# Optimization experiments

Hardware: AMD Instinct MI355X
Metric: run time of the kernel (lower is better)

Reference implementation:

```python
import jax, jax.numpy as jnp
import numpy as np

P, D, K, E, ITERS, THRESH, NCLS = 16, 384, 16, 8, 10, 0.9, 1000


def _forward(x, pw, pb, ln_g, ln_b, pos, qw, qb, kw, kb, vw, vb,
             ew, eb, nw, nb, m1w, m1b, m2w, m2b, fbw, fbb, fgw, fgb, cw, cb):
    B, C, H, W = x.shape
    Hp, Wp = H // P, W // P
    # patch embedding: conv(k=s=P) == reshape + matmul; (c, ph, pw) ordering matches conv weight layout
    xp = x.reshape(B, C, Hp, P, Wp, P).transpose(0, 2, 4, 1, 3, 5).reshape(B, Hp * Wp, C * P * P)
    patches = xp @ pw + pb                                    # [B, N, D]
    # layer norm (eps=1e-5)
    mu = patches.mean(-1, keepdims=True)
    var = patches.var(-1, keepdims=True)
    pn = (patches - mu) / jnp.sqrt(var + 1e-5) * ln_g + ln_b
    # k-means (Lloyd, fixed iters, deterministic evenly-spaced init)
    N = pn.shape[1]
    init_idx = jnp.linspace(0, N - 1, K).astype(jnp.int32)
    centers0 = pn[:, init_idx]                                # [B, K, D]
    pn_sq = jnp.sum(pn * pn, -1)                              # [B, N]

    def kstep(centers, _):
        d2 = (pn_sq[:, :, None]
              - 2.0 * jnp.einsum('bnd,bkd->bnk', pn, centers)
              + jnp.sum(centers * centers, -1)[:, None, :])   # [B, N, K]
        oh = jax.nn.one_hot(jnp.argmin(d2, -1), K, dtype=pn.dtype)
        counts = oh.sum(1)                                    # [B, K]
        new = jnp.einsum('bnk,bnd->bkd', oh, pn) / jnp.maximum(counts, 1.0)[:, :, None]
        new = jnp.where(counts[:, :, None] > 0, new, centers)
        return new, None

    clusters, _ = jax.lax.scan(kstep, centers0, None, length=ITERS)  # [B, K, D]
    # attention over clusters
    clusters = clusters + pos
    Q = clusters @ qw + qb
    Kt = clusters @ kw + kb
    V = clusters @ vw + vb
    attn = jax.nn.softmax(jnp.einsum('bqd,bkd->bqk', Q, Kt) / jnp.sqrt(jnp.float32(D)), -1)
    clusters = jnp.einsum('bqk,bkd->bqd', attn, V)
    # hypergraph laplacian
    hw = jax.nn.softmax(clusters @ ew + eb, axis=1)           # [B, K, E], softmax over nodes
    Dd = hw.sum(1)                                            # [B, E]
    Hm = hw.transpose(0, 2, 1)                                # [B, E, K]
    M = (Dd ** -0.5)[:, :, None] * Hm                         # D^{-1/2} H
    L = jnp.eye(E, dtype=clusters.dtype) - jnp.einsum('bek,bfk->bef', M, Hm)  # [B, E, E]
    L = jnp.pad(L, ((0, 0), (0, K - E), (0, K - E)))          # pad to [B, K, K]
    clusters = jnp.einsum('bij,bjd->bid', L, clusters)
    clusters = clusters @ nw + nb
    # non-linear propagation MLP (exact GELU, torch default)
    clusters = jax.nn.gelu(clusters @ m1w + m1b, approximate=False) @ m2w + m2b
    # adaptive node collapse: mask from ORIGINAL clusters, sequential in-place merges
    nrm = jnp.maximum(jnp.linalg.norm(clusters, axis=-1, keepdims=True), 1e-12)
    nc = clusters / nrm
    sim = jnp.einsum('bqd,bkd->bqk', nc, nc)
    mask_any = jnp.any(sim > THRESH, axis=0)                  # [K, K]: merge pair if ANY batch exceeds
    for i in range(K):                                        # small fixed K; matches sequential torch loop
        for j in range(i + 1, K):
            cond = mask_any[i, j]
            merged = (clusters[:, i] + clusters[:, j]) * 0.5
            clusters = clusters.at[:, i].set(jnp.where(cond, merged, clusters[:, i]))
            clusters = clusters.at[:, j].set(jnp.where(cond, merged, clusters[:, j]))
    # feedback modulation
    g = clusters.mean(1)                                      # [B, D]
    fb = g @ fbw + fbb
    gate = jax.nn.sigmoid(g @ fgw + fgb)                      # [B, 1]
    clusters = clusters + fb[:, None, :] * gate[:, None, :]
    return clusters.reshape(B, -1) @ cw + cb                  # [B, num_classes]


def setup_inputs() -> dict:
    key = jax.random.key(0)
    ks = jax.random.split(key, 16)
    Wm = lambda k, *s: jax.random.normal(k, s, jnp.float32) * 0.02
    z = lambda *s: jnp.zeros(s, jnp.float32)
    return {
        'x': jax.random.normal(ks[0], (128, 3, 224, 224), jnp.float32),
        'pw': Wm(ks[1], 3 * P * P, D), 'pb': z(D),
        'ln_g': jnp.ones((D,), jnp.float32), 'ln_b': z(D),
        'pos': Wm(ks[2], K, D),
        'qw': Wm(ks[3], D, D), 'qb': z(D),
        'kw': Wm(ks[4], D, D), 'kb': z(D),
        'vw': Wm(ks[5], D, D), 'vb': z(D),
        'ew': Wm(ks[6], D, E), 'eb': z(E),
        'nw': Wm(ks[7], D, D), 'nb': z(D),
        'm1w': Wm(ks[8], D, D), 'm1b': z(D),
        'm2w': Wm(ks[9], D, D), 'm2b': z(D),
        'fbw': Wm(ks[10], D, D), 'fbb': z(D),
        'fgw': Wm(ks[11], D, 1), 'fgb': z(1),
        'cw': Wm(ks[12], D * K, NCLS), 'cb': z(NCLS),
    }


def reference(x, pw, pb, ln_g, ln_b, pos, qw, qb, kw, kb, vw, vb,
              ew, eb, nw, nb, m1w, m1b, m2w, m2b, fbw, fbb, fgw, fgb, cw, cb):
    return _forward(x, pw, pb, ln_g, ln_b, pos, qw, qb, kw, kb, vw, vb,
                    ew, eb, nw, nb, m1w, m1b, m2w, m2b, fbw, fbb, fgw, fgb, cw, cb)
```

## Files before the change

### kernel.cpp

```cpp
#include <hip/hip_runtime.h>
#include <math.h>

#define NBATCH 128
#define NPTS   196
#define DIN    768
#define DM     384
#define KCL    16
#define NEXP   8
#define NITER  10
#define NCLS   1000

__global__ __launch_bounds__(256) void init_kernel(const float* __restrict__ cb,
                                                   float* __restrict__ out,
                                                   int* __restrict__ mask) {
    int idx = blockIdx.x * 256 + threadIdx.x;
    if (idx < NBATCH * NCLS) {
        out[idx] = cb[idx % NCLS];
    } else if (idx < NBATCH * NCLS + 256) {
        mask[idx - NBATCH * NCLS] = 0;
    }
}

#define BKP 16
__global__ __launch_bounds__(512, 4) void patch_ln_kernel(
        const float* __restrict__ x, const float* __restrict__ pw,
        const float* __restrict__ pb, const float* __restrict__ lng,
        const float* __restrict__ lnb, float* __restrict__ pn,
        float* __restrict__ pnsq) {
    __shared__ float As[BKP * 68];
    __shared__ float Ws[BKP * DM];
    const int tid = threadIdx.x;
    const int m0  = blockIdx.x * 64;
    const int rg  = tid >> 6;
    const int cg  = tid & 63;
    const int lr = (tid & 255) >> 2, kq = tid & 3;
    const int m  = m0 + lr;
    const int bi = m / NPTS, n = m - bi * NPTS;
    const int nh = n / 14, nwp = n - nh * 14;
    const float* xb = x + (size_t)bi * 150528 + (size_t)(nh * 16) * 224 + nwp * 16;

    float acc[8][6];
#pragma unroll
    for (int r = 0; r < 8; ++r)
#pragma unroll
        for (int j = 0; j < 6; ++j) acc[r][j] = 0.f;

    const float4* pw4 = (const float4*)pw;
    float4 xv = make_float4(0.f, 0.f, 0.f, 0.f);
    float4 wv0, wv1, wv2;
    if (tid < 256) {
        int k = kq * 4;
        int c = k >> 8, py = (k >> 4) & 15, px = k & 15;
        xv = *(const float4*)(xb + c * 50176 + py * 224 + px);
    }
    wv0 = pw4[tid];
    wv1 = pw4[tid + 512];
    wv2 = pw4[tid + 1024];

    for (int kc = 0; kc < DIN; kc += BKP) {
        if (tid < 256) {
            As[(kq * 4 + 0) * 68 + lr] = xv.x;
            As[(kq * 4 + 1) * 68 + lr] = xv.y;
            As[(kq * 4 + 2) * 68 + lr] = xv.z;
            As[(kq * 4 + 3) * 68 + lr] = xv.w;
        }
        ((float4*)Ws)[tid]        = wv0;
        ((float4*)Ws)[tid + 512]  = wv1;
        ((float4*)Ws)[tid + 1024] = wv2;
        __syncthreads();
        const int kn = kc + BKP;
        if (kn < DIN) {
            if (tid < 256) {
                int k = kn + kq * 4;
                int c = k >> 8, py = (k >> 4) & 15, px = k & 15;
                xv = *(const float4*)(xb + c * 50176 + py * 224 + px);
            }
            wv0 = pw4[kn * 96 + tid];
            wv1 = pw4[kn * 96 + tid + 512];
            wv2 = pw4[kn * 96 + tid + 1024];
        }
#pragma unroll 4
        for (int kk = 0; kk < BKP; ++kk) {
            float a[8];
            *(float4*)&a[0] = *(const float4*)&As[kk * 68 + rg * 8];
            *(float4*)&a[4] = *(const float4*)&As[kk * 68 + rg * 8 + 4];
            float w[6];
#pragma unroll
            for (int j = 0; j < 6; ++j) w[j] = Ws[kk * DM + cg + 64 * j];
#pragma unroll
            for (int r = 0; r < 8; ++r)
#pragma unroll
                for (int j = 0; j < 6; ++j) acc[r][j] += a[r] * w[j];
        }
        __syncthreads();
    }

    float gvv[6], bvv[6], pbv[6];
#pragma unroll
    for (int j = 0; j < 6; ++j) {
        pbv[j] = pb[cg + 64 * j];
        gvv[j] = lng[cg + 64 * j];
        bvv[j] = lnb[cg + 64 * j];
    }
#pragma unroll
    for (int r = 0; r < 8; ++r) {
        float vloc[6];
        float s = 0.f;
#pragma unroll
        for (int j = 0; j < 6; ++j) { vloc[j] = acc[r][j] + pbv[j]; s += vloc[j]; }
#pragma unroll
        for (int off = 32; off >= 1; off >>= 1) s += __shfl_xor(s, off);
        float mu = s * (1.0f / DM);
        float q = 0.f;
#pragma unroll
        for (int j = 0; j < 6; ++j) { float dd = vloc[j] - mu; q += dd * dd; }
#pragma unroll
        for (int off = 32; off >= 1; off >>= 1) q += __shfl_xor(q, off);
        float rstd = rsqrtf(q * (1.0f / DM) + 1e-5f);
        float ov[6];
        float ssq = 0.f;
#pragma unroll
        for (int j = 0; j < 6; ++j) {
            float p = (vloc[j] - mu) * rstd * gvv[j] + bvv[j];
            ov[j] = p; ssq += p * p;
        }
#pragma unroll
        for (int off = 32; off >= 1; off >>= 1) ssq += __shfl_xor(ssq, off);
        int mr = m0 + rg * 8 + r;
        float* dst = pn + (size_t)mr * DM + cg;
#pragma unroll
        for (int j = 0; j < 6; ++j) dst[64 * j] = ov[j];
        if (cg == 0) pnsq[mr] = ssq;
    }
}

#define RED8(v) { v += __shfl_xor(v, 1); v += __shfl_xor(v, 2); \
                  v += __shfl_xor(v, 4); }

__global__ __launch_bounds__(1024)
__attribute__((amdgpu_waves_per_eu(4, 4)))
void kmeans_fused_kernel(
        const float* __restrict__ pn, const float* __restrict__ pnsq,
        const float* __restrict__ pos, float* __restrict__ c0) {
    __shared__ float cs[KCL * DM];
    __shared__ float cq[KCL];
    __shared__ float spq[NPTS];
    __shared__ int   asn[256];
    __shared__ int   lst[KCL * 200];
    const int b = blockIdx.x, tid = threadIdx.x;
    const float4* pn4 = (const float4*)(pn + (size_t)b * NPTS * DM);
    float4* cs4 = (float4*)cs;

    for (int idx = tid; idx < KCL * DM / 4; idx += 1024) {
        int k = idx / 96, d4 = idx - k * 96;
        cs4[idx] = pn4[(size_t)(13 * k) * 96 + d4];
    }
    if (tid < NPTS) spq[tid] = pnsq[b * NPTS + tid];
    if (tid >= NPTS && tid < 256) asn[tid] = -1;
    __syncthreads();
    {
        const int w = tid >> 6, lane = tid & 63;
        float4 A = cs4[w * 96 + lane];
        float ss = A.x * A.x + A.y * A.y + A.z * A.z + A.w * A.w;
        if (lane < 32) {
            float4 B = cs4[w * 96 + 64 + lane];
            ss += B.x * B.x + B.y * B.y + B.z * B.z + B.w * B.w;
        }
#pragma unroll
        for (int off = 32; off >= 1; off >>= 1) ss += __shfl_xor(ss, off);
        if (lane == 0) cq[w] = ss;
    }

    const int p = tid >> 3, sub = tid & 7;
    const int p2 = p + 128;
    const bool v2 = (p2 < NPTS);
    const int p2c = v2 ? p2 : 0;
    for (int it = 0; it < NITER; ++it) {
        __syncthreads();
        float acc0[KCL], acc1[KCL];
#pragma unroll
        for (int k = 0; k < KCL; ++k) { acc0[k] = 0.f; acc1[k] = 0.f; }
#pragma unroll 2
        for (int i = 0; i < 12; ++i) {
            const int d4 = sub + 8 * i;
            float4 a0 = pn4[(size_t)p * 96 + d4];
            float4 a1 = pn4[(size_t)p2c * 96 + d4];
#pragma unroll
            for (int k = 0; k < KCL; ++k) {
                float4 c = *(const float4*)&cs[k * DM + d4 * 4];
                acc0[k] += a0.x * c.x + a0.y * c.y + a0.z * c.z + a0.w * c.w;
                acc1[k] += a1.x * c.x + a1.y * c.y + a1.z * c.z + a1.w * c.w;
            }
        }
#pragma unroll
        for (int k = 0; k < KCL; ++k) {
            float a = acc0[k]; RED8(a); acc0[k] = a;
            float d = acc1[k]; RED8(d); acc1[k] = d;
        }
        if (sub == 0) {
            {
                float mp = spq[p];
                float best = (mp - 2.0f * acc0[0]) + cq[0]; int bk = 0;
#pragma unroll
                for (int k = 1; k < KCL; ++k) {
                    float v = (mp - 2.0f * acc0[k]) + cq[k];
                    if (v < best) { best = v; bk = k; }
                }
                asn[p] = bk;
            }
            if (v2) {
                float mp = spq[p2];
                float best = (mp - 2.0f * acc1[0]) + cq[0]; int bk = 0;
#pragma unroll
                for (int k = 1; k < KCL; ++k) {
                    float v = (mp - 2.0f * acc1[k]) + cq[k];
                    if (v < best) { best = v; bk = k; }
                }
                asn[p2] = bk;
            }
        }
        __syncthreads();
        {
            const int w = tid >> 6, lane = tid & 63;
            int cnt = 0;
#pragma unroll
            for (int ch = 0; ch < 4; ++ch) {
                int a = asn[ch * 64 + lane];
                unsigned long long mm = __ballot(a == w);
                if (a == w) {
                    int r = __popcll(mm & ((1ull << lane) - 1ull));
                    lst[w * 200 + cnt + r] = ch * 64 + lane;
                }
                cnt += __popcll(mm);
            }
            float4 sA = make_float4(0.f, 0.f, 0.f, 0.f);
            float4 sB = make_float4(0.f, 0.f, 0.f, 0.f);
            int i = 0;
            for (; i + 4 <= cnt; i += 4) {
                int n0 = lst[w * 200 + i];
                int n1 = lst[w * 200 + i + 1];
                int n2 = lst[w * 200 + i + 2];
                int n3 = lst[w * 200 + i + 3];
                float4 vA0 = pn4[(size_t)n0 * 96 + lane];
                float4 vA1 = pn4[(size_t)n1 * 96 + lane];
                float4 vA2 = pn4[(size_t)n2 * 96 + lane];
                float4 vA3 = pn4[(size_t)n3 * 96 + lane];
                float4 vB0, vB1, vB2, vB3;
                if (lane < 32) {
                    vB0 = pn4[(size_t)n0 * 96 + 64 + lane];
                    vB1 = pn4[(size_t)n1 * 96 + 64 + lane];
                    vB2 = pn4[(size_t)n2 * 96 + 64 + lane];
                    vB3 = pn4[(size_t)n3 * 96 + 64 + lane];
                }
                sA.x += vA0.x; sA.y += vA0.y; sA.z += vA0.z; sA.w += vA0.w;
                sA.x += vA1.x; sA.y += vA1.y; sA.z += vA1.z; sA.w += vA1.w;
                sA.x += vA2.x; sA.y += vA2.y; sA.z += vA2.z; sA.w += vA2.w;
                sA.x += vA3.x; sA.y += vA3.y; sA.z += vA3.z; sA.w += vA3.w;
                if (lane < 32) {
                    sB.x += vB0.x; sB.y += vB0.y; sB.z += vB0.z; sB.w += vB0.w;
                    sB.x += vB1.x; sB.y += vB1.y; sB.z += vB1.z; sB.w += vB1.w;
                    sB.x += vB2.x; sB.y += vB2.y; sB.z += vB2.z; sB.w += vB2.w;
                    sB.x += vB3.x; sB.y += vB3.y; sB.z += vB3.z; sB.w += vB3.w;
                }
            }
            for (; i < cnt; ++i) {
                int nn = lst[w * 200 + i];
                float4 vA = pn4[(size_t)nn * 96 + lane];
                sA.x += vA.x; sA.y += vA.y; sA.z += vA.z; sA.w += vA.w;
                if (lane < 32) {
                    float4 vB = pn4[(size_t)nn * 96 + 64 + lane];
                    sB.x += vB.x; sB.y += vB.y; sB.z += vB.z; sB.w += vB.w;
                }
            }
            float4 nA, nB = make_float4(0.f, 0.f, 0.f, 0.f);
            if (cnt > 0) {
                float inv = 1.0f / (float)cnt;
                nA.x = sA.x * inv; nA.y = sA.y * inv; nA.z = sA.z * inv; nA.w = sA.w * inv;
                if (lane < 32) {
                    nB.x = sB.x * inv; nB.y = sB.y * inv; nB.z = sB.z * inv; nB.w = sB.w * inv;
                }
            } else {
                nA = cs4[w * 96 + lane];
                if (lane < 32) nB = cs4[w * 96 + 64 + lane];
            }
            cs4[w * 96 + lane] = nA;
            if (lane < 32) cs4[w * 96 + 64 + lane] = nB;
            float ss = nA.x * nA.x + nA.y * nA.y + nA.z * nA.z + nA.w * nA.w
                     + nB.x * nB.x + nB.y * nB.y + nB.z * nB.z + nB.w * nB.w;
#pragma unroll
            for (int off = 32; off >= 1; off >>= 1) ss += __shfl_xor(ss, off);
            if (lane == 0) cq[w] = ss;
        }
    }
    __syncthreads();
    const float4* pos4 = (const float4*)pos;
    float4* c0b = (float4*)(c0 + (size_t)b * KCL * DM);
    for (int idx = tid; idx < KCL * DM / 4; idx += 1024) {
        float4 cv = cs4[idx];
        float4 pv = pos4[idx];
        cv.x += pv.x; cv.y += pv.y; cv.z += pv.z; cv.w += pv.w;
        c0b[idx] = cv;
    }
}

__global__ __launch_bounds__(256) void gemm_qkv_kernel(
        const float* __restrict__ A,
        const float* __restrict__ qw, const float* __restrict__ kw,
        const float* __restrict__ vw,
        const float* __restrict__ qb, const float* __restrict__ kb,
        const float* __restrict__ vb,
        float* __restrict__ Q, float* __restrict__ K, float* __restrict__ V) {
    __shared__ float As[32 * 32];
    __shared__ float Ws[3][32 * 128];
    const int n0 = blockIdx.x * 128;
    const int m0 = blockIdx.y * 32;
    const int tid = threadIdx.x;
    const int rg = tid >> 5, cg = tid & 31;
    const int arow = tid >> 3, akg = tid & 7;
    const float* W[3] = {qw, kw, vw};

    float acc[3][4][4];
#pragma unroll
    for (int g = 0; g < 3; ++g)
#pragma unroll
        for (int r = 0; r < 4; ++r)
#pragma unroll
            for (int j = 0; j < 4; ++j) acc[g][r][j] = 0.f;

    for (int kc = 0; kc < DM; kc += 32) {
        float4 av = *(const float4*)(A + (size_t)(m0 + arow) * DM + kc + akg * 4);
        As[(akg * 4 + 0) * 32 + arow] = av.x;
        As[(akg * 4 + 1) * 32 + arow] = av.y;
        As[(akg * 4 + 2) * 32 + arow] = av.z;
        As[(akg * 4 + 3) * 32 + arow] = av.w;
#pragma unroll
        for (int g = 0; g < 3; ++g)
#pragma unroll
            for (int t = 0; t < 4; ++t) {
                int s = tid + t * 256;
                int kk = s >> 5, c4i = s & 31;
                *(float4*)&Ws[g][kk * 128 + c4i * 4] =
                    *(const float4*)(W[g] + (size_t)(kc + kk) * DM + n0 + c4i * 4);
            }
        __syncthreads();
#pragma unroll 8
        for (int kk = 0; kk < 32; ++kk) {
            float4 a = *(const float4*)&As[kk * 32 + rg * 4];
            float ar[4] = {a.x, a.y, a.z, a.w};
#pragma unroll
            for (int g = 0; g < 3; ++g) {
                float4 w = *(const float4*)&Ws[g][kk * 128 + cg * 4];
                float wr[4] = {w.x, w.y, w.z, w.w};
#pragma unroll
                for (int r = 0; r < 4; ++r)
#pragma unroll
                    for (int j = 0; j < 4; ++j) acc[g][r][j] += ar[r] * wr[j];
            }
        }
        __syncthreads();
    }
    const float* B[3] = {qb, kb, vb};
    float* O[3] = {Q, K, V};
#pragma unroll
    for (int g = 0; g < 3; ++g) {
        float4 bv = *(const float4*)(B[g] + n0 + cg * 4);
        float bvr[4] = {bv.x, bv.y, bv.z, bv.w};
#pragma unroll
        for (int r = 0; r < 4; ++r) {
            float o[4];
#pragma unroll
            for (int j = 0; j < 4; ++j) o[j] = acc[g][r][j] + bvr[j];
            *(float4*)(O[g] + (size_t)(m0 + rg * 4 + r) * DM + n0 + cg * 4) =
                *(float4*)&o[0];
        }
    }
}

template <int ACT>
__global__ __launch_bounds__(256) void gemm_kernel(
        const float* __restrict__ A, const float* __restrict__ W,
        const float* __restrict__ bias, float* __restrict__ out,
        int M, int N, int Kd) {
    __shared__ float As[32 * 32];
    __shared__ float Ws[32 * 128];
    const int n0 = blockIdx.x * 128;
    const int m0 = blockIdx.y * 32;
    const int tid = threadIdx.x;
    const int rg = tid >> 5, cg = tid & 31;
    const int arow = tid >> 3, akg = tid & 7;
    float acc[4][4];
#pragma unroll
    for (int r = 0; r < 4; ++r)
#pragma unroll
        for (int j = 0; j < 4; ++j) acc[r][j] = 0.f;

    for (int kc = 0; kc < Kd; kc += 32) {
        float4 av = *(const float4*)(A + (size_t)(m0 + arow) * Kd + kc + akg * 4);
        As[(akg * 4 + 0) * 32 + arow] = av.x;
        As[(akg * 4 + 1) * 32 + arow] = av.y;
        As[(akg * 4 + 2) * 32 + arow] = av.z;
        As[(akg * 4 + 3) * 32 + arow] = av.w;
#pragma unroll
        for (int t = 0; t < 4; ++t) {
            int s = tid + t * 256;
            int kk = s >> 5, c4i = s & 31;
            *(float4*)&Ws[kk * 128 + c4i * 4] =
                *(const float4*)(W + (size_t)(kc + kk) * N + n0 + c4i * 4);
        }
        __syncthreads();
#pragma unroll 16
        for (int kk = 0; kk < 32; ++kk) {
            float4 a = *(const float4*)&As[kk * 32 + rg * 4];
            float4 w = *(const float4*)&Ws[kk * 128 + cg * 4];
            float ar[4] = {a.x, a.y, a.z, a.w};
            float wr[4] = {w.x, w.y, w.z, w.w};
#pragma unroll
            for (int r = 0; r < 4; ++r)
#pragma unroll
                for (int j = 0; j < 4; ++j) acc[r][j] += ar[r] * wr[j];
        }
        __syncthreads();
    }
    float4 bv = *(const float4*)(bias + n0 + cg * 4);
    float bvr[4] = {bv.x, bv.y, bv.z, bv.w};
#pragma unroll
    for (int r = 0; r < 4; ++r) {
        float o[4];
#pragma unroll
        for (int j = 0; j < 4; ++j) {
            float v = acc[r][j] + bvr[j];
            if (ACT == 1) v = 0.5f * v * (1.0f + erff(v * 0.70710678118654752440f));
            o[j] = v;
        }
        *(float4*)(out + (size_t)(m0 + rg * 4 + r) * N + n0 + cg * 4) = *(float4*)&o[0];
    }
}

__global__ __launch_bounds__(256) void attn_spectral_kernel(
        const float* __restrict__ Qg, const float* __restrict__ Kg,
        const float* __restrict__ Vg, const float* __restrict__ ew,
        const float* __restrict__ eb, float* __restrict__ c2) {
    __shared__ float Qs[KCL * 388];
    __shared__ float Ks[KCL * 388];
    __shared__ float ewt[NEXP * 388];
    __shared__ float Ss[KCL * 17];
    __shared__ float hws[KCL * 9];
    __shared__ float rds[NEXP];
    __shared__ float Ls[NEXP * NEXP];
    const int b = blockIdx.x, tid = threadIdx.x;
    for (int idx = tid; idx < KCL * DM; idx += 256) {
        int i = idx / DM, d = idx - i * DM;
        size_t g = (size_t)b * KCL * DM + idx;
        Qs[i * 388 + d] = Qg[g];
        Ks[i * 388 + d] = Kg[g];
    }
    for (int idx = tid; idx < DM * NEXP; idx += 256) {
        int d = idx >> 3, e = idx & 7;
        ewt[e * 388 + d] = ew[idx];
    }
    __syncthreads();
    {
        int i = tid >> 4, j = tid & 15;
        float acc = 0.f;
        for (int d = 0; d < DM; d += 4) {
            float4 q = *(const float4*)&Qs[i * 388 + d];
            float4 k = *(const float4*)&Ks[j * 388 + d];
            acc += q.x * k.x + q.y * k.y + q.z * k.z + q.w * k.w;
        }
        float s = acc / sqrtf((float)DM);
        float mx = s;
#pragma unroll
        for (int off = 8; off >= 1; off >>= 1) mx = fmaxf(mx, __shfl_xor(mx, off));
        float p = expf(s - mx);
        float sm = p;
#pragma unroll
        for (int off = 8; off >= 1; off >>= 1) sm += __shfl_xor(sm, off);
        Ss[i * 17 + j] = p / sm;
    }
    __syncthreads();
    for (int idx = tid; idx < KCL * DM; idx += 256) {
        int i = idx / DM, d = idx - i * DM;
        Ks[i * 388 + d] = Vg[(size_t)b * KCL * DM + idx];
    }
    __syncthreads();
    for (int idx = tid; idx < KCL * DM; idx += 256) {
        int i = idx / DM, d = idx - i * DM;
        float acc = 0.f;
#pragma unroll
        for (int j = 0; j < KCL; ++j) acc += Ss[i * 17 + j] * Ks[j * 388 + d];
        Qs[i * 388 + d] = acc;
    }
    __syncthreads();
    if (tid < 128) {
        int e = tid >> 4, i = tid & 15;
        float l = 0.f;
        for (int d4 = 0; d4 < DM / 4; ++d4) {
            float4 q = *(const float4*)&Qs[i * 388 + d4 * 4];
            float4 w = *(const float4*)&ewt[e * 388 + d4 * 4];
            l += q.x * w.x + q.y * w.y + q.z * w.z + q.w * w.w;
        }
        l += eb[e];
        float mx = l;
#pragma unroll
        for (int off = 8; off >= 1; off >>= 1) mx = fmaxf(mx, __shfl_xor(mx, off));
        float p = expf(l - mx);
        float sm = p;
#pragma unroll
        for (int off = 8; off >= 1; off >>= 1) sm += __shfl_xor(sm, off);
        float h = p / sm;
        hws[i * 9 + e] = h;
        float sd = h;
#pragma unroll
        for (int off = 8; off >= 1; off >>= 1) sd += __shfl_xor(sd, off);
        if (i == 0) rds[e] = 1.0f / sqrtf(sd);
    }
    __syncthreads();
    if (tid < 64) {
        int e = tid >> 3, f = tid & 7;
        float gsum = 0.f;
#pragma unroll
        for (int k = 0; k < KCL; ++k) gsum += hws[k * 9 + e] * hws[k * 9 + f];
        Ls[e * 8 + f] = ((e == f) ? 1.0f : 0.0f) - rds[e] * gsum;
    }
    __syncthreads();
    for (int idx = tid; idx < KCL * DM; idx += 256) {
        int i = idx / DM, d = idx - i * DM;
        float acc = 0.f;
        if (i < NEXP) {
#pragma unroll
            for (int j = 0; j < NEXP; ++j) acc += Ls[i * 8 + j] * Qs[j * 388 + d];
        }
        c2[(size_t)b * KCL * DM + idx] = acc;
    }
}

__global__ __launch_bounds__(256) void simmask_kernel(const float* __restrict__ c4,
                                                      int* __restrict__ mask) {
    __shared__ float Cs[KCL * 388];
    __shared__ float rns[KCL];
    const int b = blockIdx.x, tid = threadIdx.x;
    for (int idx = tid; idx < KCL * DM; idx += 256) {
        int i = idx / DM, d = idx - i * DM;
        Cs[i * 388 + d] = c4[(size_t)b * KCL * DM + idx];
    }
    __syncthreads();
    {
        int i = tid >> 4, s = tid & 15;
        float ss = 0.f;
        for (int t = 0; t < 24; ++t) { float v = Cs[i * 388 + s + 16 * t]; ss += v * v; }
#pragma unroll
        for (int off = 8; off >= 1; off >>= 1) ss += __shfl_xor(ss, off);
        if (s == 0) rns[i] = 1.0f / fmaxf(sqrtf(ss), 1e-12f);
    }
    __syncthreads();
    for (int idx = tid; idx < KCL * DM; idx += 256) {
        int i = idx / DM, d = idx - i * DM;
        Cs[i * 388 + d] *= rns[i];
    }
    __syncthreads();
    {
        int i = tid >> 4, j = tid & 15;
        if (j > i) {
            float dp = 0.f;
            for (int d = 0; d < DM; d += 4) {
                float4 a = *(const float4*)&Cs[i * 388 + d];
                float4 c = *(const float4*)&Cs[j * 388 + d];
                dp += a.x * c.x + a.y * c.y + a.z * c.z + a.w * c.w;
            }
            if (dp > 0.9f) atomicOr(&mask[i * KCL + j], 1);
        }
    }
}

__global__ __launch_bounds__(256) void merge_fb_kernel(
        const float* __restrict__ c4, const int* __restrict__ mask,
        const float* __restrict__ fbw, const float* __restrict__ fbb,
        const float* __restrict__ fgw, const float* __restrict__ fgb,
        float* __restrict__ c5) {
    __shared__ int   mk[256];
    __shared__ float gs[DM];
    __shared__ float wred[3];
    __shared__ float gatev;
    const int b = blockIdx.x, tid = threadIdx.x;
    mk[tid] = mask[tid];
    const bool act = tid < 192;
    const int t = tid;
    float2 v[KCL];
    if (act) {
#pragma unroll
        for (int i = 0; i < KCL; ++i)
            v[i] = *(const float2*)(c4 + (size_t)b * KCL * DM + i * DM + 2 * t);
    }
    __syncthreads();
    if (act) {
#pragma unroll
        for (int i = 0; i < KCL; ++i)
#pragma unroll
            for (int j = i + 1; j < KCL; ++j)
                if (mk[i * KCL + j]) {
                    float mx = 0.5f * (v[i].x + v[j].x);
                    float my = 0.5f * (v[i].y + v[j].y);
                    v[i].x = mx; v[i].y = my; v[j].x = mx; v[j].y = my;
                }
    }
    float2 gv = {0.f, 0.f};
    if (act) {
#pragma unroll
        for (int i = 0; i < KCL; ++i) { gv.x += v[i].x; gv.y += v[i].y; }
        gv.x *= 0.0625f; gv.y *= 0.0625f;
        gs[2 * t] = gv.x; gs[2 * t + 1] = gv.y;
    }
    float pg = act ? (gv.x * fgw[2 * t] + gv.y * fgw[2 * t + 1]) : 0.f;
#pragma unroll
    for (int off = 32; off >= 1; off >>= 1) pg += __shfl_xor(pg, off);
    if (act && (tid & 63) == 0) wred[tid >> 6] = pg;
    __syncthreads();
    if (tid == 0) {
        float d = wred[0] + wred[1] + wred[2] + fgb[0];
        gatev = 1.0f / (1.0f + expf(-d));
    }
    __syncthreads();
    if (act) {
        float fx = fbb[2 * t], fy = fbb[2 * t + 1];
        for (int j = 0; j < DM; ++j) {
            float gj = gs[j];
            const float2 w = *(const float2*)(fbw + (size_t)j * DM + 2 * t);
            fx += gj * w.x; fy += gj * w.y;
        }
        float gt = gatev;
#pragma unroll
        for (int i = 0; i < KCL; ++i) {
            float2 o = {v[i].x + fx * gt, v[i].y + fy * gt};
            *(float2*)(c5 + (size_t)b * KCL * DM + i * DM + 2 * t) = o;
        }
    }
}

__global__ __launch_bounds__(256) void cls_kernel(const float* __restrict__ A,
                                                  const float* __restrict__ Wt,
                                                  float* __restrict__ out) {
    __shared__ float As[32 * 32];
    __shared__ float Ws[32 * 128];
    const int n0 = blockIdx.x * 128;
    const int m0 = blockIdx.y * 32;
    const int k0 = blockIdx.z * 768;
    const int tid = threadIdx.x;
    const int rg = tid >> 5, cg = tid & 31;
    const int arow = tid >> 3, akg = tid & 7;
    float acc[4][4];
#pragma unroll
    for (int r = 0; r < 4; ++r)
#pragma unroll
        for (int j = 0; j < 4; ++j) acc[r][j] = 0.f;

    for (int kc = k0; kc < k0 + 768; kc += 32) {
        float4 av = *(const float4*)(A + (size_t)(m0 + arow) * (KCL * DM) + kc + akg * 4);
        As[(akg * 4 + 0) * 32 + arow] = av.x;
        As[(akg * 4 + 1) * 32 + arow] = av.y;
        As[(akg * 4 + 2) * 32 + arow] = av.z;
        As[(akg * 4 + 3) * 32 + arow] = av.w;
#pragma unroll
        for (int ti = 0; ti < 4; ++ti) {
            int s = tid + ti * 256;
            int kk = s >> 5, c4i = s & 31;
            int col = n0 + c4i * 4;
            float4 wv = make_float4(0.f, 0.f, 0.f, 0.f);
            if (col < NCLS) wv = *(const float4*)(Wt + (size_t)(kc + kk) * NCLS + col);
            *(float4*)&Ws[kk * 128 + c4i * 4] = wv;
        }
        __syncthreads();
#pragma unroll 16
        for (int kk = 0; kk < 32; ++kk) {
            float4 a = *(const float4*)&As[kk * 32 + rg * 4];
            float4 w = *(const float4*)&Ws[kk * 128 + cg * 4];
            float ar[4] = {a.x, a.y, a.z, a.w};
            float wr[4] = {w.x, w.y, w.z, w.w};
#pragma unroll
            for (int r = 0; r < 4; ++r)
#pragma unroll
                for (int j = 0; j < 4; ++j) acc[r][j] += ar[r] * wr[j];
        }
        __syncthreads();
    }
    int col = n0 + cg * 4;
    if (col < NCLS) {
#pragma unroll
        for (int r = 0; r < 4; ++r) {
            int row = m0 + rg * 4 + r;
#pragma unroll
            for (int j = 0; j < 4; ++j)
                atomicAdd(&out[(size_t)row * NCLS + col + j], acc[r][j]);
        }
    }
}

extern "C" void kernel_launch(void* const* d_in, const int* in_sizes, int n_in,
                              void* d_out, int out_size, void* d_ws, size_t ws_size,
                              hipStream_t stream) {
    const float* x   = (const float*)d_in[0];
    const float* pw  = (const float*)d_in[1];
    const float* pb  = (const float*)d_in[2];
    const float* lng = (const float*)d_in[3];
    const float* lnb = (const float*)d_in[4];
    const float* pos = (const float*)d_in[5];
    const float* qw  = (const float*)d_in[6];
    const float* qb  = (const float*)d_in[7];
    const float* kw  = (const float*)d_in[8];
    const float* kb  = (const float*)d_in[9];
    const float* vw  = (const float*)d_in[10];
    const float* vb  = (const float*)d_in[11];
    const float* ew  = (const float*)d_in[12];
    const float* eb  = (const float*)d_in[13];
    const float* nw  = (const float*)d_in[14];
    const float* nb  = (const float*)d_in[15];
    const float* m1w = (const float*)d_in[16];
    const float* m1b = (const float*)d_in[17];
    const float* m2w = (const float*)d_in[18];
    const float* m2b = (const float*)d_in[19];
    const float* fbw = (const float*)d_in[20];
    const float* fbb = (const float*)d_in[21];
    const float* fgw = (const float*)d_in[22];
    const float* fgb = (const float*)d_in[23];
    const float* cw  = (const float*)d_in[24];
    const float* cb  = (const float*)d_in[25];
    float* out = (float*)d_out;
    float* ws  = (float*)d_ws;

    float* pn_   = ws;
    float* pnsq_ = ws + 9633792;
    float* c0_   = ws + 9658880;
    float* Q_    = ws + 10445312;
    float* K_    = ws + 11231744;
    float* V_    = ws + 12018176;
    float* c2_   = ws + 12804608;
    int*   mask_ = (int*)(ws + 13591040);
    float* c3_ = Q_;
    float* h_  = K_;
    float* c4_ = V_;
    float* c5_ = c0_;

    init_kernel<<<501, 256, 0, stream>>>(cb, out, mask_);
    patch_ln_kernel<<<392, 512, 0, stream>>>(x, pw, pb, lng, lnb, pn_, pnsq_);

    kmeans_fused_kernel<<<NBATCH, 1024, 0, stream>>>(pn_, pnsq_, pos, c0_);

    gemm_qkv_kernel<<<dim3(3, 64), 256, 0, stream>>>(c0_, qw, kw, vw, qb, kb, vb,
                                                     Q_, K_, V_);
    attn_spectral_kernel<<<NBATCH, 256, 0, stream>>>(Q_, K_, V_, ew, eb, c2_);
    gemm_kernel<0><<<dim3(3, 64), 256, 0, stream>>>(c2_, nw, nb, c3_, 2048, DM, DM);
    gemm_kernel<1><<<dim3(3, 64), 256, 0, stream>>>(c3_, m1w, m1b, h_, 2048, DM, DM);
    gemm_kernel<0><<<dim3(3, 64), 256, 0, stream>>>(h_, m2w, m2b, c4_, 2048, DM, DM);
    simmask_kernel<<<NBATCH, 256, 0, stream>>>(c4_, mask_);
    merge_fb_kernel<<<NBATCH, 256, 0, stream>>>(c4_, mask_, fbw, fbb, fgw, fgb, c5_);
    cls_kernel<<<dim3(8, 4, 8), 256, 0, stream>>>(c5_, cw, out);
}
```

Baseline: 915.0 us.

## Retile patch GEMM to 32-row blocks and give k-means threads four points each

The patch-embedding GEMM and layernorm kernel now uses 256-thread blocks covering 32 rows each, launching twice as many blocks. It also drops the register double-buffered prefetch in favour of direct load, store and sync per K chunk. The k-means assignment step now runs on 512 threads, each handling four points, so every centroid value read from shared memory is reused across more points. The trade-off is less load/compute overlap in the patch GEMM and idle threads during assignment, in exchange for more blocks to spread across CUs and less shared-memory traffic.

```diff
diff --git a/kernel.cpp b/kernel.cpp
--- a/kernel.cpp
+++ b/kernel.cpp
@@ -22,18 +22,18 @@
 }
 
 #define BKP 16
-__global__ __launch_bounds__(512, 4) void patch_ln_kernel(
+__global__ __launch_bounds__(256) void patch_ln_kernel(
         const float* __restrict__ x, const float* __restrict__ pw,
         const float* __restrict__ pb, const float* __restrict__ lng,
         const float* __restrict__ lnb, float* __restrict__ pn,
         float* __restrict__ pnsq) {
-    __shared__ float As[BKP * 68];
+    __shared__ float As[BKP * 36];
     __shared__ float Ws[BKP * DM];
     const int tid = threadIdx.x;
-    const int m0  = blockIdx.x * 64;
+    const int m0  = blockIdx.x * 32;
     const int rg  = tid >> 6;
     const int cg  = tid & 63;
-    const int lr = (tid & 255) >> 2, kq = tid & 3;
+    const int lr = (tid & 127) >> 2, kq = tid & 3;
     const int m  = m0 + lr;
     const int bi = m / NPTS, n = m - bi * NPTS;
     const int nh = n / 14, nwp = n - nh * 14;
@@ -46,44 +46,27 @@
         for (int j = 0; j < 6; ++j) acc[r][j] = 0.f;
 
     const float4* pw4 = (const float4*)pw;
-    float4 xv = make_float4(0.f, 0.f, 0.f, 0.f);
-    float4 wv0, wv1, wv2;
-    if (tid < 256) {
-        int k = kq * 4;
-        int c = k >> 8, py = (k >> 4) & 15, px = k & 15;
-        xv = *(const float4*)(xb + c * 50176 + py * 224 + px);
-    }
-    wv0 = pw4[tid];
-    wv1 = pw4[tid + 512];
-    wv2 = pw4[tid + 1024];
-
     for (int kc = 0; kc < DIN; kc += BKP) {
-        if (tid < 256) {
-            As[(kq * 4 + 0) * 68 + lr] = xv.x;
-            As[(kq * 4 + 1) * 68 + lr] = xv.y;
-            As[(kq * 4 + 2) * 68 + lr] = xv.z;
-            As[(kq * 4 + 3) * 68 + lr] = xv.w;
-        }
-        ((float4*)Ws)[tid]        = wv0;
-        ((float4*)Ws)[tid + 512]  = wv1;
-        ((float4*)Ws)[tid + 1024] = wv2;
-        __syncthreads();
-        const int kn = kc + BKP;
-        if (kn < DIN) {
-            if (tid < 256) {
-                int k = kn + kq * 4;
-                int c = k >> 8, py = (k >> 4) & 15, px = k & 15;
-                xv = *(const float4*)(xb + c * 50176 + py * 224 + px);
-            }
-            wv0 = pw4[kn * 96 + tid];
-            wv1 = pw4[kn * 96 + tid + 512];
-            wv2 = pw4[kn * 96 + tid + 1024];
-        }
+        if (tid < 128) {
+            int k = kc + kq * 4;
+            int c = k >> 8, py = (k >> 4) & 15, px = k & 15;
+            float4 xv = *(const float4*)(xb + c * 50176 + py * 224 + px);
+            As[(kq * 4 + 0) * 36 + lr] = xv.x;
+            As[(kq * 4 + 1) * 36 + lr] = xv.y;
+            As[(kq * 4 + 2) * 36 + lr] = xv.z;
+            As[(kq * 4 + 3) * 36 + lr] = xv.w;
+        }
+#pragma unroll
+        for (int t = 0; t < 6; ++t) {
+            int s = tid + t * 256;
+            ((float4*)Ws)[s] = pw4[kc * 96 + s];
+        }
+        __syncthreads();
 #pragma unroll 4
         for (int kk = 0; kk < BKP; ++kk) {
             float a[8];
-            *(float4*)&a[0] = *(const float4*)&As[kk * 68 + rg * 8];
-            *(float4*)&a[4] = *(const float4*)&As[kk * 68 + rg * 8 + 4];
+            *(float4*)&a[0] = *(const float4*)&As[kk * 36 + rg * 8];
+            *(float4*)&a[4] = *(const float4*)&As[kk * 36 + rg * 8 + 4];
             float w[6];
 #pragma unroll
             for (int j = 0; j < 6; ++j) w[j] = Ws[kk * DM + cg + 64 * j];
@@ -171,52 +154,82 @@
         if (lane == 0) cq[w] = ss;
     }
 
-    const int p = tid >> 3, sub = tid & 7;
-    const int p2 = p + 128;
-    const bool v2 = (p2 < NPTS);
-    const int p2c = v2 ? p2 : 0;
+    const int slot = tid >> 3, sub = tid & 7;
+    const int q0 = slot, q1 = slot + 64, q2 = slot + 128;
+    const bool h3 = (slot < 4);
+    const int q3 = h3 ? slot + 192 : 0;
     for (int it = 0; it < NITER; ++it) {
         __syncthreads();
-        float acc0[KCL], acc1[KCL];
-#pragma unroll
-        for (int k = 0; k < KCL; ++k) { acc0[k] = 0.f; acc1[k] = 0.f; }
+        if (tid < 512) {
+            float acc0[KCL], acc1[KCL], acc2[KCL], acc3[KCL];
+#pragma unroll
+            for (int k = 0; k < KCL; ++k) {
+                acc0[k] = 0.f; acc1[k] = 0.f; acc2[k] = 0.f; acc3[k] = 0.f;
+            }
 #pragma unroll 2
-        for (int i = 0; i < 12; ++i) {
-            const int d4 = sub + 8 * i;
-            float4 a0 = pn4[(size_t)p * 96 + d4];
-            float4 a1 = pn4[(size_t)p2c * 96 + d4];
+            for (int i = 0; i < 12; ++i) {
+                const int d4 = sub + 8 * i;
+                float4 a0 = pn4[(size_t)q0 * 96 + d4];
+                float4 a1 = pn4[(size_t)q1 * 96 + d4];
+                float4 a2 = pn4[(size_t)q2 * 96 + d4];
+                float4 a3 = pn4[(size_t)q3 * 96 + d4];
+#pragma unroll
+                for (int k = 0; k < KCL; ++k) {
+                    float4 c = *(const float4*)&cs[k * DM + d4 * 4];
+                    acc0[k] += a0.x * c.x + a0.y * c.y + a0.z * c.z + a0.w * c.w;
+                    acc1[k] += a1.x * c.x + a1.y * c.y + a1.z * c.z + a1.w * c.w;
+                    acc2[k] += a2.x * c.x + a2.y * c.y + a2.z * c.z + a2.w * c.w;
+                    acc3[k] += a3.x * c.x + a3.y * c.y + a3.z * c.z + a3.w * c.w;
+                }
+            }
 #pragma unroll
             for (int k = 0; k < KCL; ++k) {
-                float4 c = *(const float4*)&cs[k * DM + d4 * 4];
-                acc0[k] += a0.x * c.x + a0.y * c.y + a0.z * c.z + a0.w * c.w;
-                acc1[k] += a1.x * c.x + a1.y * c.y + a1.z * c.z + a1.w * c.w;
-            }
-        }
-#pragma unroll
-        for (int k = 0; k < KCL; ++k) {
-            float a = acc0[k]; RED8(a); acc0[k] = a;
-            float d = acc1[k]; RED8(d); acc1[k] = d;
-        }
-        if (sub == 0) {
-            {
-                float mp = spq[p];
-                float best = (mp - 2.0f * acc0[0]) + cq[0]; int bk = 0;
-#pragma unroll
-                for (int k = 1; k < KCL; ++k) {
-                    float v = (mp - 2.0f * acc0[k]) + cq[k];
-                    if (v < best) { best = v; bk = k; }
-                }
-                asn[p] = bk;
-            }
-            if (v2) {
-                float mp = spq[p2];
-                float best = (mp - 2.0f * acc1[0]) + cq[0]; int bk = 0;
-#pragma unroll
-                for (int k = 1; k < KCL; ++k) {
-                    float v = (mp - 2.0f * acc1[k]) + cq[k];
-                    if (v < best) { best = v; bk = k; }
-                }
-                asn[p2] = bk;
+                float a = acc0[k]; RED8(a); acc0[k] = a;
+                float d = acc1[k]; RED8(d); acc1[k] = d;
+                float e = acc2[k]; RED8(e); acc2[k] = e;
+                float f = acc3[k]; RED8(f); acc3[k] = f;
+            }
+            if (sub == 0) {
+                {
+                    float mp = spq[q0];
+                    float best = (mp - 2.0f * acc0[0]) + cq[0]; int bk = 0;
+#pragma unroll
+                    for (int k = 1; k < KCL; ++k) {
+                        float v = (mp - 2.0f * acc0[k]) + cq[k];
+                        if (v < best) { best = v; bk = k; }
+                    }
+                    asn[q0] = bk;
+                }
+                {
+                    float mp = spq[q1];
+                    float best = (mp - 2.0f * acc1[0]) + cq[0]; int bk = 0;
+#pragma unroll
+                    for (int k = 1; k < KCL; ++k) {
+                        float v = (mp - 2.0f * acc1[k]) + cq[k];
+                        if (v < best) { best = v; bk = k; }
+                    }
+                    asn[q1] = bk;
+                }
+                {
+                    float mp = spq[q2];
+                    float best = (mp - 2.0f * acc2[0]) + cq[0]; int bk = 0;
+#pragma unroll
+                    for (int k = 1; k < KCL; ++k) {
+                        float v = (mp - 2.0f * acc2[k]) + cq[k];
+                        if (v < best) { best = v; bk = k; }
+                    }
+                    asn[q2] = bk;
+                }
+                if (h3) {
+                    float mp = spq[q3];
+                    float best = (mp - 2.0f * acc3[0]) + cq[0]; int bk = 0;
+#pragma unroll
+                    for (int k = 1; k < KCL; ++k) {
+                        float v = (mp - 2.0f * acc3[k]) + cq[k];
+                        if (v < best) { best = v; bk = k; }
+                    }
+                    asn[q3] = bk;
+                }
             }
         }
         __syncthreads();
@@ -740,7 +753,7 @@
     float* c5_ = c0_;
 
     init_kernel<<<501, 256, 0, stream>>>(cb, out, mask_);
-    patch_ln_kernel<<<392, 512, 0, stream>>>(x, pw, pb, lng, lnb, pn_, pnsq_);
+    patch_ln_kernel<<<784, 256, 0, stream>>>(x, pw, pb, lng, lnb, pn_, pnsq_);
 
     kmeans_fused_kernel<<<NBATCH, 1024, 0, stream>>>(pn_, pnsq_, pos, c0_);
 
```

Result: slower. 3.264 ms (+256.8%).

## Restructure k-means distance loop into 4-point by 8-cluster register tiles

Applied to the files above, without the earlier changes.

The k-means assignment step now has 16 lanes per point slot, each covering four points and processing the 16 clusters in two halves of eight. Partial dot products are reduced with a 16-lane shuffle and written to a shared-memory table, and a separate pass does the argmin per point. The aim is to reuse each loaded centroid float4 across four points and to lower register pressure, dropping the fixed waves-per-EU attribute. The cost is an extra barrier, extra shared memory for the dot table, and more shuffle reductions.

```diff
diff --git a/kernel.cpp b/kernel.cpp
--- a/kernel.cpp
+++ b/kernel.cpp
@@ -134,11 +134,10 @@
     }
 }
 
-#define RED8(v) { v += __shfl_xor(v, 1); v += __shfl_xor(v, 2); \
-                  v += __shfl_xor(v, 4); }
+#define RED16v(v) { v += __shfl_xor(v, 1); v += __shfl_xor(v, 2); \
+                    v += __shfl_xor(v, 4); v += __shfl_xor(v, 8); }
 
 __global__ __launch_bounds__(1024)
-__attribute__((amdgpu_waves_per_eu(4, 4)))
 void kmeans_fused_kernel(
         const float* __restrict__ pn, const float* __restrict__ pnsq,
         const float* __restrict__ pos, float* __restrict__ c0) {
@@ -147,6 +146,7 @@
     __shared__ float spq[NPTS];
     __shared__ int   asn[256];
     __shared__ int   lst[KCL * 200];
+    __shared__ float dts[256][17];
     const int b = blockIdx.x, tid = threadIdx.x;
     const float4* pn4 = (const float4*)(pn + (size_t)b * NPTS * DM);
     float4* cs4 = (float4*)cs;
@@ -171,53 +171,62 @@
         if (lane == 0) cq[w] = ss;
     }
 
-    const int p = tid >> 3, sub = tid & 7;
-    const int p2 = p + 128;
-    const bool v2 = (p2 < NPTS);
-    const int p2c = v2 ? p2 : 0;
+    const int slot = tid >> 4, sub = tid & 15;
+    const int q0 = slot, q1 = slot + 64, q2 = slot + 128;
+    const bool h3 = (slot < 4);
+    const int q3 = h3 ? slot + 192 : 0;
     for (int it = 0; it < NITER; ++it) {
         __syncthreads();
-        float acc0[KCL], acc1[KCL];
-#pragma unroll
-        for (int k = 0; k < KCL; ++k) { acc0[k] = 0.f; acc1[k] = 0.f; }
-#pragma unroll 2
-        for (int i = 0; i < 12; ++i) {
-            const int d4 = sub + 8 * i;
-            float4 a0 = pn4[(size_t)p * 96 + d4];
-            float4 a1 = pn4[(size_t)p2c * 96 + d4];
-#pragma unroll
-            for (int k = 0; k < KCL; ++k) {
-                float4 c = *(const float4*)&cs[k * DM + d4 * 4];
-                acc0[k] += a0.x * c.x + a0.y * c.y + a0.z * c.z + a0.w * c.w;
-                acc1[k] += a1.x * c.x + a1.y * c.y + a1.z * c.z + a1.w * c.w;
-            }
-        }
-#pragma unroll
-        for (int k = 0; k < KCL; ++k) {
-            float a = acc0[k]; RED8(a); acc0[k] = a;
-            float d = acc1[k]; RED8(d); acc1[k] = d;
-        }
-        if (sub == 0) {
-            {
-                float mp = spq[p];
-                float best = (mp - 2.0f * acc0[0]) + cq[0]; int bk = 0;
-#pragma unroll
-                for (int k = 1; k < KCL; ++k) {
-                    float v = (mp - 2.0f * acc0[k]) + cq[k];
-                    if (v < best) { best = v; bk = k; }
+#pragma unroll 1
+        for (int kh = 0; kh < 2; ++kh) {
+            float acc[4][8];
+#pragma unroll
+            for (int k8 = 0; k8 < 8; ++k8) {
+                acc[0][k8] = 0.f; acc[1][k8] = 0.f;
+                acc[2][k8] = 0.f; acc[3][k8] = 0.f;
+            }
+#pragma unroll 1
+            for (int i = 0; i < 6; ++i) {
+                const int d4 = sub + 16 * i;
+                float4 a0 = pn4[(size_t)q0 * 96 + d4];
+                float4 a1 = pn4[(size_t)q1 * 96 + d4];
+                float4 a2 = pn4[(size_t)q2 * 96 + d4];
+                float4 a3 = pn4[(size_t)q3 * 96 + d4];
+#pragma unroll
+                for (int k8 = 0; k8 < 8; ++k8) {
+                    const float4 c = *(const float4*)&cs[(kh * 8 + k8) * DM + d4 * 4];
+                    acc[0][k8] += a0.x * c.x + a0.y * c.y + a0.z * c.z + a0.w * c.w;
+                    acc[1][k8] += a1.x * c.x + a1.y * c.y + a1.z * c.z + a1.w * c.w;
+                    acc[2][k8] += a2.x * c.x + a2.y * c.y + a2.z * c.z + a2.w * c.w;
+                    acc[3][k8] += a3.x * c.x + a3.y * c.y + a3.z * c.z + a3.w * c.w;
                 }
-                asn[p] = bk;
-            }
-            if (v2) {
-                float mp = spq[p2];
-                float best = (mp - 2.0f * acc1[0]) + cq[0]; int bk = 0;
-#pragma unroll
-                for (int k = 1; k < KCL; ++k) {
-                    float v = (mp - 2.0f * acc1[k]) + cq[k];
-                    if (v < best) { best = v; bk = k; }
+            }
+#pragma unroll
+            for (int k8 = 0; k8 < 8; ++k8) {
+                float v0 = acc[0][k8]; RED16v(v0);
+                float v1 = acc[1][k8]; RED16v(v1);
+                float v2 = acc[2][k8]; RED16v(v2);
+                float v3 = acc[3][k8]; RED16v(v3);
+                if (sub == 0) {
+                    const int kk = kh * 8 + k8;
+                    dts[q0][kk] = v0;
+                    dts[q1][kk] = v1;
+                    dts[q2][kk] = v2;
+                    if (h3) dts[q3][kk] = v3;
                 }
-                asn[p2] = bk;
-            }
+            }
+        }
+        __syncthreads();
+        if (tid < NPTS) {
+            const float mp = spq[tid];
+            float best = (mp - 2.0f * dts[tid][0]) + cq[0];
+            int bk = 0;
+#pragma unroll
+            for (int k = 1; k < KCL; ++k) {
+                float v = (mp - 2.0f * dts[tid][k]) + cq[k];
+                if (v < best) { best = v; bk = k; }
+            }
+            asn[tid] = bk;
         }
         __syncthreads();
         {
```

Result: slower. 984.0 us (+7.5%).

## Fuse node, MLP1 (GELU) and MLP2 GEMMs into one row-blocked kernel

Applied to the files above, without the earlier changes.

Replaces three separate 2048x384x384 GEMM launches with a single kernel in which each block owns 8 rows and keeps the intermediate activations in shared memory across all three stages. This removes two global round-trips of intermediates and two launches. In exchange, each block re-streams all three full weight matrices, and there are 256 blocks with small row tiles, so weight traffic through L2 grows. It also adds an unroll pragma to the fb loop in merge_fb.

```diff
diff --git a/kernel.cpp b/kernel.cpp
--- a/kernel.cpp
+++ b/kernel.cpp
@@ -376,63 +376,79 @@
     }
 }
 
-template <int ACT>
-__global__ __launch_bounds__(256) void gemm_kernel(
-        const float* __restrict__ A, const float* __restrict__ W,
-        const float* __restrict__ bias, float* __restrict__ out,
-        int M, int N, int Kd) {
-    __shared__ float As[32 * 32];
-    __shared__ float Ws[32 * 128];
-    const int n0 = blockIdx.x * 128;
-    const int m0 = blockIdx.y * 32;
+__global__ __launch_bounds__(256) void gemm3_fused_kernel(
+        const float* __restrict__ c2,
+        const float* __restrict__ nw,  const float* __restrict__ nb,
+        const float* __restrict__ m1w, const float* __restrict__ m1b,
+        const float* __restrict__ m2w, const float* __restrict__ m2b,
+        float* __restrict__ c4) {
+    __shared__ float A0[8][388];
+    __shared__ float T1[8][388];
+    __shared__ float Ws[16 * DM];
     const int tid = threadIdx.x;
-    const int rg = tid >> 5, cg = tid & 31;
-    const int arow = tid >> 3, akg = tid & 7;
-    float acc[4][4];
-#pragma unroll
-    for (int r = 0; r < 4; ++r)
-#pragma unroll
-        for (int j = 0; j < 4; ++j) acc[r][j] = 0.f;
-
-    for (int kc = 0; kc < Kd; kc += 32) {
-        float4 av = *(const float4*)(A + (size_t)(m0 + arow) * Kd + kc + akg * 4);
-        As[(akg * 4 + 0) * 32 + arow] = av.x;
-        As[(akg * 4 + 1) * 32 + arow] = av.y;
-        As[(akg * 4 + 2) * 32 + arow] = av.z;
-        As[(akg * 4 + 3) * 32 + arow] = av.w;
-#pragma unroll
-        for (int t = 0; t < 4; ++t) {
-            int s = tid + t * 256;
-            int kk = s >> 5, c4i = s & 31;
-            *(float4*)&Ws[kk * 128 + c4i * 4] =
-                *(const float4*)(W + (size_t)(kc + kk) * N + n0 + c4i * 4);
-        }
-        __syncthreads();
-#pragma unroll 16
-        for (int kk = 0; kk < 32; ++kk) {
-            float4 a = *(const float4*)&As[kk * 32 + rg * 4];
-            float4 w = *(const float4*)&Ws[kk * 128 + cg * 4];
-            float ar[4] = {a.x, a.y, a.z, a.w};
-            float wr[4] = {w.x, w.y, w.z, w.w};
-#pragma unroll
-            for (int r = 0; r < 4; ++r)
-#pragma unroll
-                for (int j = 0; j < 4; ++j) acc[r][j] += ar[r] * wr[j];
-        }
-        __syncthreads();
-    }
-    float4 bv = *(const float4*)(bias + n0 + cg * 4);
-    float bvr[4] = {bv.x, bv.y, bv.z, bv.w};
-#pragma unroll
-    for (int r = 0; r < 4; ++r) {
-        float o[4];
-#pragma unroll
-        for (int j = 0; j < 4; ++j) {
-            float v = acc[r][j] + bvr[j];
-            if (ACT == 1) v = 0.5f * v * (1.0f + erff(v * 0.70710678118654752440f));
-            o[j] = v;
-        }
-        *(float4*)(out + (size_t)(m0 + rg * 4 + r) * N + n0 + cg * 4) = *(float4*)&o[0];
+    const int r0  = blockIdx.x * 8;
+    const int rg  = tid >> 6;
+    const int cg  = tid & 63;
+    const float4* c24 = (const float4*)(c2 + (size_t)r0 * DM);
+
+#pragma unroll
+    for (int t = 0; t < 3; ++t) {
+        int s = tid + t * 256;
+        int rr = s / 96, d4 = s - rr * 96;
+        *(float4*)&A0[rr][d4 * 4] = c24[s];
+    }
+    __syncthreads();
+
+    const float4* w4[3] = {(const float4*)nw, (const float4*)m1w,
+                           (const float4*)m2w};
+    const float* bias[3] = {nb, m1b, m2b};
+
+#pragma unroll 1
+    for (int st = 0; st < 3; ++st) {
+        const float (*SRC)[388] = (st == 1) ? (const float(*)[388])T1
+                                            : (const float(*)[388])A0;
+        float acc[2][6];
+#pragma unroll
+        for (int r = 0; r < 2; ++r)
+#pragma unroll
+            for (int j = 0; j < 6; ++j) acc[r][j] = 0.f;
+        for (int kc = 0; kc < DM; kc += 16) {
+#pragma unroll
+            for (int t = 0; t < 6; ++t) {
+                int s = tid + t * 256;
+                ((float4*)Ws)[s] = w4[st][kc * 96 + s];
+            }
+            __syncthreads();
+#pragma unroll 4
+            for (int kk = 0; kk < 16; ++kk) {
+                float a0 = SRC[rg * 2 + 0][kc + kk];
+                float a1 = SRC[rg * 2 + 1][kc + kk];
+                float w[6];
+#pragma unroll
+                for (int j = 0; j < 6; ++j) w[j] = Ws[kk * DM + cg + 64 * j];
+#pragma unroll
+                for (int j = 0; j < 6; ++j) {
+                    acc[0][j] += a0 * w[j];
+                    acc[1][j] += a1 * w[j];
+                }
+            }
+            __syncthreads();
+        }
+#pragma unroll
+        for (int r = 0; r < 2; ++r) {
+#pragma unroll
+            for (int j = 0; j < 6; ++j) {
+                float v = acc[r][j] + bias[st][cg + 64 * j];
+                if (st == 1)
+                    v = 0.5f * v * (1.0f + erff(v * 0.70710678118654752440f));
+                if (st == 0)      T1[rg * 2 + r][cg + 64 * j] = v;
+                else if (st == 1) A0[rg * 2 + r][cg + 64 * j] = v;
+                else {
+                    c4[(size_t)(r0 + rg * 2 + r) * DM + cg + 64 * j] = v;
+                }
+            }
+        }
+        __syncthreads();
     }
 }
 
@@ -622,6 +638,7 @@
     __syncthreads();
     if (act) {
         float fx = fbb[2 * t], fy = fbb[2 * t + 1];
+#pragma unroll 4
         for (int j = 0; j < DM; ++j) {
             float gj = gs[j];
             const float2 w = *(const float2*)(fbw + (size_t)j * DM + 2 * t);
@@ -734,8 +751,6 @@
     float* V_    = ws + 12018176;
     float* c2_   = ws + 12804608;
     int*   mask_ = (int*)(ws + 13591040);
-    float* c3_ = Q_;
-    float* h_  = K_;
     float* c4_ = V_;
     float* c5_ = c0_;
 
@@ -747,9 +762,8 @@
     gemm_qkv_kernel<<<dim3(3, 64), 256, 0, stream>>>(c0_, qw, kw, vw, qb, kb, vb,
                                                      Q_, K_, V_);
     attn_spectral_kernel<<<NBATCH, 256, 0, stream>>>(Q_, K_, V_, ew, eb, c2_);
-    gemm_kernel<0><<<dim3(3, 64), 256, 0, stream>>>(c2_, nw, nb, c3_, 2048, DM, DM);
-    gemm_kernel<1><<<dim3(3, 64), 256, 0, stream>>>(c3_, m1w, m1b, h_, 2048, DM, DM);
-    gemm_kernel<0><<<dim3(3, 64), 256, 0, stream>>>(h_, m2w, m2b, c4_, 2048, DM, DM);
+    gemm3_fused_kernel<<<256, 256, 0, stream>>>(c2_, nw, nb, m1w, m1b,
+                                                m2w, m2b, c4_);
     simmask_kernel<<<NBATCH, 256, 0, stream>>>(c4_, mask_);
     merge_fb_kernel<<<NBATCH, 256, 0, stream>>>(c4_, mask_, fbw, fbb, fgw, fgb, c5_);
     cls_kernel<<<dim3(8, 4, 8), 256, 0, stream>>>(c5_, cw, out);
```

Result: slower. 1.086 ms (+18.7%).
